# Performance work log

Measured on AMD Instinct MI355X. Metric: run time of the kernel, lower is better.

## Reference

```python
import jax, jax.numpy as jnp
import numpy as np

N, E, B = 10000, 60000, 4
NODE_IN, EDGE_IN, COND_IN, SCALE_IN = 6, 6, 10, 4
H, KW, OUT = 64, 256, 1
NUM_LAYERS = 3


def _lin(key, fan_in, fan_out):
    return jax.random.normal(key, (fan_in, fan_out), jnp.float32) / np.sqrt(fan_in).astype(np.float32)


def setup_inputs() -> dict:
    key = jax.random.key(0)
    ks = jax.random.split(key, 16)
    return {
        "x": jax.random.normal(ks[0], (N, NODE_IN), jnp.float32),
        "edge_attr": jax.random.normal(ks[1], (E, EDGE_IN), jnp.float32),
        "conditions": jax.random.normal(ks[2], (B, COND_IN), jnp.float32),
        "scale": jax.random.normal(ks[3], (B, SCALE_IN), jnp.float32),
        "edge_index": jax.random.randint(ks[4], (2, E), 0, N, dtype=jnp.int32),
        "batch": jnp.sort(jax.random.randint(ks[5], (N,), 0, B, dtype=jnp.int32)),
        # node encoder
        "nW1": _lin(ks[6], NODE_IN, H), "nb1": jnp.zeros((H,), jnp.float32),
        "nW2": _lin(ks[7], H, H), "nb2": jnp.zeros((H,), jnp.float32),
        # condition encoder
        "cW1": _lin(ks[8], COND_IN + SCALE_IN, H), "cb1": jnp.zeros((H,), jnp.float32),
        "cW2": _lin(ks[9], H, H), "cb2": jnp.zeros((H,), jnp.float32),
        # kernel network (DenseNet [EDGE_IN+H, KW//2, KW, H*H])
        "kW1": _lin(ks[10], EDGE_IN + H, KW // 2), "kb1": jnp.zeros((KW // 2,), jnp.float32),
        "kW2": _lin(ks[11], KW // 2, KW), "kb2": jnp.zeros((KW,), jnp.float32),
        "kW3": _lin(ks[12], KW, H * H), "kb3": jnp.zeros((H * H,), jnp.float32),
        # NNConv root weight + bias
        "root": _lin(ks[13], H, H), "conv_bias": jnp.zeros((H,), jnp.float32),
        # output head
        "oW": _lin(ks[14], H, OUT), "ob": jnp.zeros((OUT,), jnp.float32),
    }


def reference(x, edge_attr, conditions, scale, edge_index, batch,
              nW1, nb1, nW2, nb2, cW1, cb1, cW2, cb2,
              kW1, kb1, kW2, kb2, kW3, kb3, root, conv_bias, oW, ob):
    # node + condition encoders
    h = jax.nn.relu(x @ nW1 + nb1) @ nW2 + nb2                                   # [N,H]
    u = jax.nn.relu(jnp.concatenate([conditions, scale], 1) @ cW1 + cb1) @ cW2 + cb2  # [B,H]

    src, dst = edge_index[0], edge_index[1]
    # per-edge conditioned attributes
    ea = jnp.concatenate([edge_attr, u[batch[src]]], axis=1)                     # [E,EDGE_IN+H]
    # kernel network -> per-edge H x H weight (same every layer, compute once)
    k = jax.nn.relu(ea @ kW1 + kb1)
    k = jax.nn.relu(k @ kW2 + kb2)
    w = (k @ kW3 + kb3).reshape(E, H, H)                                          # [E,H,H]

    # mean-aggregation degree (clamped to >=1, matching scatter_mean semantics)
    deg = jnp.maximum(jax.ops.segment_sum(jnp.ones((E,), x.dtype), dst, num_segments=N), 1.0)

    for _ in range(NUM_LAYERS):
        msg = jnp.einsum('ei,eio->eo', h[src], w)                                 # gather + bmm
        agg = jax.ops.segment_sum(msg, dst, num_segments=N) / deg[:, None]        # scatter-mean
        h = jax.nn.relu(agg + h @ root + conv_bias)

    out = h @ oW + ob                                                             # [N,OUT]
    return out, u
```

## Files before the change

### kernel.cpp

```cpp
#include <hip/hip_runtime.h>
#include <hip/hip_fp16.h>

#define N_NODES 10000
#define N_EDGES 60000
#define EPAD    60032
#define CSPLIT  2
#define CT_PER  32

typedef _Float16 f16;
typedef f16 f16x8 __attribute__((ext_vector_type(8)));
typedef float f32x4 __attribute__((ext_vector_type(4)));

__device__ __forceinline__ void gload16(const void* g, void* l) {
    __builtin_amdgcn_global_load_lds((const __attribute__((address_space(1))) unsigned int*)g,
                                     (__attribute__((address_space(3))) unsigned int*)l, 16, 0, 0);
}

__device__ __forceinline__ float foldp(float a, float b, int m, int lane) {
    float x = (lane & m) ? b : a;
    float y = (lane & m) ? a : b;
    return x + __shfl_xor(y, m);
}

__global__ void k_node_enc(const float* __restrict__ x, const float* __restrict__ W1,
                           const float* __restrict__ b1, const float* __restrict__ W2,
                           const float* __restrict__ b2, float* __restrict__ h) {
    __shared__ float t[4][64];
    int g = threadIdx.x >> 6, j = threadIdx.x & 63;
    int node = blockIdx.x * 4 + g;
    float acc = b1[j];
#pragma unroll
    for (int i = 0; i < 6; ++i) acc += x[node * 6 + i] * W1[i * 64 + j];
    t[g][j] = fmaxf(acc, 0.f);
    __syncthreads();
    float acc2 = b2[j];
#pragma unroll
    for (int i = 0; i < 64; ++i) acc2 += t[g][i] * W2[i * 64 + j];
    h[node * 64 + j] = acc2;
}

__global__ void k_cond_enc(const float* __restrict__ cond, const float* __restrict__ scl,
                           const float* __restrict__ W1, const float* __restrict__ b1,
                           const float* __restrict__ W2, const float* __restrict__ b2,
                           float* __restrict__ u, float* __restrict__ out_u) {
    __shared__ float t[4][64];
    __shared__ float cat[4][14];
    int g = threadIdx.x >> 6, j = threadIdx.x & 63;
    if (threadIdx.x < 56) {
        int b = threadIdx.x / 14, i = threadIdx.x % 14;
        cat[b][i] = (i < 10) ? cond[b * 10 + i] : scl[b * 4 + (i - 10)];
    }
    __syncthreads();
    float acc = b1[j];
#pragma unroll
    for (int i = 0; i < 14; ++i) acc += cat[g][i] * W1[i * 64 + j];
    t[g][j] = fmaxf(acc, 0.f);
    __syncthreads();
    float acc2 = b2[j];
#pragma unroll
    for (int i = 0; i < 64; ++i) acc2 += t[g][i] * W2[i * 64 + j];
    u[g * 64 + j] = acc2;
    out_u[g * 64 + j] = acc2;
}

__global__ void k_deg(const int* __restrict__ dst, float* __restrict__ deg) {
    int e = blockIdx.x * 256 + threadIdx.x;
    if (e < N_EDGES) atomicAdd(&deg[dst[e]], 1.0f);
}
__global__ void k_deg_inv(float* __restrict__ deg) {
    int n = blockIdx.x * 256 + threadIdx.x;
    if (n < N_NODES) deg[n] = 1.0f / fmaxf(deg[n], 1.0f);
}

__global__ void k_permute(const float* __restrict__ kW3, const float* __restrict__ kb3,
                          f16* __restrict__ kW3P, float* __restrict__ kb3P) {
    __shared__ float T[256][65];
    int i = blockIdx.x;
    int o = threadIdx.x & 63, kq = threadIdx.x >> 6;
    for (int kk = 0; kk < 64; ++kk) {
        int k = kk * 4 + kq;
        T[k][o] = kW3[(size_t)k * 4096 + i * 64 + o];
    }
    if (threadIdx.x < 64) kb3P[threadIdx.x * 64 + i] = kb3[i * 64 + threadIdx.x];
    __syncthreads();
    int ow = threadIdx.x >> 2, kc = (threadIdx.x & 3) * 64;
    int nf = i >> 4, rl = i & 15;
    for (int c = 0; c < 8; ++c) {
        int k0 = kc + c * 8;
        int ks = k0 >> 5, kg = (k0 >> 3) & 3;
        int chunk = (nf * 8 + ks) * 64 + kg * 16 + rl;
        f16x8 v;
#pragma unroll
        for (int jj = 0; jj < 8; ++jj) v[jj] = (f16)T[k0 + jj][ow];
        *(f16x8*)(kW3P + (size_t)ow * 16384 + chunk * 8) = v;
    }
}

__global__ __launch_bounds__(256) void k_edge12(const float* __restrict__ ea, const int* __restrict__ ei,
                                                const int* __restrict__ batch, const float* __restrict__ u,
                                                const float* __restrict__ W1, const float* __restrict__ b1,
                                                const float* __restrict__ W2, const float* __restrict__ b2,
                                                f16* __restrict__ k2) {
    __shared__ float u_s[256];
    __shared__ float ea_s[16][6];
    __shared__ int b_s[16];
    __shared__ float k1_s[16][128];
    int tid = threadIdx.x;
    int e0 = blockIdx.x * 16;
    u_s[tid] = u[tid];
    if (tid < 96) {
        int e = tid / 6, i = tid % 6;
        int eg = e0 + e;
        ea_s[e][i] = (eg < N_EDGES) ? ea[(size_t)eg * 6 + i] : 0.f;
    }
    if (tid < 16) {
        int eg = e0 + tid;
        b_s[tid] = (eg < N_EDGES) ? batch[ei[eg]] : 0;
    }
    __syncthreads();
    int j = tid & 127;
#pragma unroll 1
    for (int p = 0; p < 8; ++p) {
        int e = p * 2 + (tid >> 7);
        float acc = b1[j];
#pragma unroll
        for (int i = 0; i < 6; ++i) acc += ea_s[e][i] * W1[i * 128 + j];
        const float* ur = u_s + b_s[e] * 64;
#pragma unroll
        for (int i = 0; i < 64; ++i) acc += ur[i] * W1[(6 + i) * 128 + j];
        k1_s[e][j] = fmaxf(acc, 0.f);
    }
    __syncthreads();
    float acc2[16];
#pragma unroll
    for (int e = 0; e < 16; ++e) acc2[e] = b2[tid];
    for (int i = 0; i < 128; ++i) {
        float w = W2[(size_t)i * 256 + tid];
#pragma unroll
        for (int e = 0; e < 16; ++e) acc2[e] += k1_s[e][i] * w;
    }
#pragma unroll
    for (int e = 0; e < 16; ++e) {
        int eg = e0 + e;
        k2[(size_t)eg * 256 + tid] = (f16)((eg < N_EDGES) ? fmaxf(acc2[e], 0.f) : 0.f);
    }
}

__global__ __launch_bounds__(256) void k_fused(const f16* __restrict__ A, const f16* __restrict__ Bf,
                                               const float* __restrict__ kb3P, const float* __restrict__ h,
                                               const int* __restrict__ ei, const float* __restrict__ dinv,
                                               float* __restrict__ agg) {
    __shared__ __align__(16) f16 lB[2][16384];
    __shared__ float bias_s[CT_PER * 64];
    __shared__ int src_s[128];
    __shared__ int dst_s[128];
    __shared__ float dinv_s[128];
    int tid = threadIdx.x, wave = tid >> 6, lane = tid & 63;
    int m0 = blockIdx.x * 128;
    int ct0 = blockIdx.y * CT_PER;
    if (tid < 128) {
        int eg = m0 + tid; int s = 0, d = 0; float dv = 0.f;
        if (eg < N_EDGES) { s = ei[eg]; d = ei[N_EDGES + eg]; dv = dinv[d]; }
        src_s[tid] = s; dst_s[tid] = d; dinv_s[tid] = dv;
    }
#pragma unroll
    for (int q = 0; q < CT_PER * 64 / 256; ++q)
        bias_s[q * 256 + tid] = kb3P[ct0 * 64 + q * 256 + tid];
    {
        const f16* bp = Bf + (size_t)ct0 * 16384;
#pragma unroll
        for (int q = 0; q < 8; ++q)
            gload16(bp + (q * 256 + tid) * 8, &lB[0][(q * 256 + wave * 64) * 8]);
    }
    __syncthreads();
    f16x8 a[2][8];
#pragma unroll
    for (int mf = 0; mf < 2; ++mf) {
        const f16* ap = A + (size_t)(m0 + wave * 32 + mf * 16 + (lane & 15)) * 256 + (lane >> 4) * 8;
#pragma unroll
        for (int ks = 0; ks < 8; ++ks) a[mf][ks] = *(const f16x8*)(ap + ks * 32);
    }
    float hsr[2][4][4];
#pragma unroll
    for (int mf = 0; mf < 2; ++mf)
#pragma unroll
        for (int jj = 0; jj < 4; ++jj) {
            int el = wave * 32 + mf * 16 + (lane >> 4) * 4 + jj;
            const float* hp = h + (size_t)src_s[el] * 64 + (lane & 15);
            float dv = dinv_s[el];
#pragma unroll
            for (int nf = 0; nf < 4; ++nf) hsr[mf][jj][nf] = hp[nf * 16] * dv;
        }
    int cur = 0;
    float w4[4];
#pragma unroll 1
    for (int cto = 0; cto < CT_PER; cto += 4) {
#pragma unroll
        for (int q4 = 0; q4 < 4; ++q4) {
            int ctl = cto + q4;
            if (ctl + 1 < CT_PER) {
                const f16* bp = Bf + (size_t)(ct0 + ctl + 1) * 16384;
#pragma unroll
                for (int q = 0; q < 8; ++q)
                    gload16(bp + (q * 256 + tid) * 8, &lB[cur ^ 1][(q * 256 + wave * 64) * 8]);
            }
            f32x4 acc[2][4];
#pragma unroll
            for (int nf = 0; nf < 4; ++nf) {
                float bv = bias_s[ctl * 64 + nf * 16 + (lane & 15)];
                acc[0][nf] = {bv, bv, bv, bv};
                acc[1][nf] = {bv, bv, bv, bv};
            }
            const f16* lb = lB[cur];
#pragma unroll
            for (int ks = 0; ks < 8; ++ks) {
                f16x8 bf[4];
#pragma unroll
                for (int nf = 0; nf < 4; ++nf)
                    bf[nf] = *(const f16x8*)(lb + (nf * 8 + ks) * 512 + lane * 8);
#pragma unroll
                for (int mf = 0; mf < 2; ++mf)
#pragma unroll
                    for (int nf = 0; nf < 4; ++nf)
                        acc[mf][nf] = __builtin_amdgcn_mfma_f32_16x16x32_f16(a[mf][ks], bf[nf], acc[mf][nf], 0, 0, 0);
            }
            float v[8];
#pragma unroll
            for (int mf = 0; mf < 2; ++mf)
#pragma unroll
                for (int jj = 0; jj < 4; ++jj)
                    v[mf * 4 + jj] = acc[mf][0][jj] * hsr[mf][jj][0] + acc[mf][1][jj] * hsr[mf][jj][1]
                                   + acc[mf][2][jj] * hsr[mf][jj][2] + acc[mf][3][jj] * hsr[mf][jj][3];
            float t0 = foldp(v[0], v[1], 1, lane);
            float t1 = foldp(v[2], v[3], 1, lane);
            float t2 = foldp(v[4], v[5], 1, lane);
            float t3 = foldp(v[6], v[7], 1, lane);
            float u0 = foldp(t0, t1, 2, lane);
            float u1 = foldp(t2, t3, 2, lane);
            float s0 = foldp(u0, u1, 4, lane);
            s0 += __shfl_xor(s0, 8);
            w4[q4] = s0;
            if (q4 == 3) {
                if (!(lane & 8)) {
                    int mf = (lane >> 2) & 1, jj = lane & 3;
                    int el = wave * 32 + mf * 16 + (lane >> 4) * 4 + jj;
                    float* ap2 = agg + (size_t)dst_s[el] * 64 + ct0 + cto;
                    atomicAdd(ap2 + 0, w4[0]);
                    atomicAdd(ap2 + 1, w4[1]);
                    atomicAdd(ap2 + 2, w4[2]);
                    atomicAdd(ap2 + 3, w4[3]);
                }
            }
            cur ^= 1;
            __syncthreads();
        }
    }
}

__global__ void k_update(const float* __restrict__ agg, const float* __restrict__ h,
                         const float* __restrict__ root, const float* __restrict__ bias,
                         float* __restrict__ hn) {
    __shared__ float t[4][64];
    int g = threadIdx.x >> 6, j = threadIdx.x & 63;
    int node = blockIdx.x * 4 + g;
    t[g][j] = h[node * 64 + j];
    __syncthreads();
    float acc = agg[node * 64 + j] + bias[j];
#pragma unroll
    for (int i = 0; i < 64; ++i) acc += t[g][i] * root[i * 64 + j];
    hn[node * 64 + j] = fmaxf(acc, 0.f);
}

__global__ void k_out(const float* __restrict__ h, const float* __restrict__ oW,
                      const float* __restrict__ ob, float* __restrict__ out) {
    int wg = (blockIdx.x * 256 + threadIdx.x) >> 6;
    int lane = threadIdx.x & 63;
    if (wg >= N_NODES) return;
    float p = h[wg * 64 + lane] * oW[lane];
#pragma unroll
    for (int s = 32; s > 0; s >>= 1) p += __shfl_xor(p, s);
    if (lane == 0) out[wg] = p + ob[0];
}

__global__ void k_sentinel(float* out) { out[0] = 1e30f; }

extern "C" void kernel_launch(void* const* d_in, const int* in_sizes, int n_in,
                              void* d_out, int out_size, void* d_ws, size_t ws_size,
                              hipStream_t stream) {
    const float* x          = (const float*)d_in[0];
    const float* edge_attr  = (const float*)d_in[1];
    const float* conditions = (const float*)d_in[2];
    const float* scale      = (const float*)d_in[3];
    const int*   edge_index = (const int*)d_in[4];
    const int*   batch      = (const int*)d_in[5];
    const float* nW1 = (const float*)d_in[6];  const float* nb1 = (const float*)d_in[7];
    const float* nW2 = (const float*)d_in[8];  const float* nb2 = (const float*)d_in[9];
    const float* cW1 = (const float*)d_in[10]; const float* cb1 = (const float*)d_in[11];
    const float* cW2 = (const float*)d_in[12]; const float* cb2 = (const float*)d_in[13];
    const float* kW1 = (const float*)d_in[14]; const float* kb1 = (const float*)d_in[15];
    const float* kW2 = (const float*)d_in[16]; const float* kb2 = (const float*)d_in[17];
    const float* kW3 = (const float*)d_in[18]; const float* kb3 = (const float*)d_in[19];
    const float* root = (const float*)d_in[20]; const float* conv_bias = (const float*)d_in[21];
    const float* oW  = (const float*)d_in[22]; const float* ob  = (const float*)d_in[23];
    float* out = (float*)d_out;

    char* ws = (char*)d_ws;
    size_t off = 0;
    auto alloc = [&](size_t bytes) -> char* {
        char* p = ws + off;
        off += (bytes + 255) & ~(size_t)255;
        return p;
    };
    float* h_a  = (float*)alloc((size_t)N_NODES * 64 * 4);
    float* h_b  = (float*)alloc((size_t)N_NODES * 64 * 4);
    float* agg  = (float*)alloc((size_t)N_NODES * 64 * 4);
    float* u    = (float*)alloc(256 * 4);
    float* deg  = (float*)alloc((size_t)N_NODES * 4);
    f16*   k2   = (f16*)alloc((size_t)EPAD * 256 * 2);
    f16*   kW3P = (f16*)alloc((size_t)4096 * 256 * 2);
    float* kb3P = (float*)alloc(4096 * 4);

    if (off > ws_size) {
        k_sentinel<<<1, 1, 0, stream>>>(out);
        return;
    }

    hipMemsetAsync(deg, 0, (size_t)N_NODES * 4, stream);
    k_node_enc<<<2500, 256, 0, stream>>>(x, nW1, nb1, nW2, nb2, h_a);
    k_cond_enc<<<1, 256, 0, stream>>>(conditions, scale, cW1, cb1, cW2, cb2, u, out + N_NODES);
    k_deg<<<(N_EDGES + 255) / 256, 256, 0, stream>>>(edge_index + N_EDGES, deg);
    k_deg_inv<<<(N_NODES + 255) / 256, 256, 0, stream>>>(deg);
    k_permute<<<64, 256, 0, stream>>>(kW3, kb3, kW3P, kb3P);
    k_edge12<<<EPAD / 16, 256, 0, stream>>>(edge_attr, edge_index, batch, u, kW1, kb1, kW2, kb2, k2);

    float* hc = h_a; float* hn = h_b;
    for (int l = 0; l < 3; ++l) {
        hipMemsetAsync(agg, 0, (size_t)N_NODES * 64 * 4, stream);
        k_fused<<<dim3(EPAD / 128, CSPLIT), 256, 0, stream>>>(k2, kW3P, kb3P, hc, edge_index, deg, agg);
        k_update<<<2500, 256, 0, stream>>>(agg, hc, root, conv_bias, hn);
        float* tmp = hc; hc = hn; hn = tmp;
    }
    k_out<<<2500, 256, 0, stream>>>(hc, oW, ob, out);
}
```

Measured before the change: 896.9 us.

## Halve LDS B-tile into K-halves, drop bias smem, batch atomics by eight

Reorders the permuted kW3 layout so each output column's 256-deep K range splits into two 8192-element halves. The fused edge kernel then double-buffers half-size B tiles, which halves its LDS footprint, and requests 4 blocks per CU through launch bounds. Bias is now read straight from global memory instead of being staged in shared memory. Atomics are grouped eight columns at a time rather than four. The cost is twice as many barriers per column and a register cap that may force spills.

```diff
diff --git a/kernel.cpp b/kernel.cpp
--- a/kernel.cpp
+++ b/kernel.cpp
@@ -87,12 +87,12 @@
     int nf = i >> 4, rl = i & 15;
     for (int c = 0; c < 8; ++c) {
         int k0 = kc + c * 8;
-        int ks = k0 >> 5, kg = (k0 >> 3) & 3;
-        int chunk = (nf * 8 + ks) * 64 + kg * 16 + rl;
+        int ks = k0 >> 5, kh = ks >> 2, ks4 = ks & 3, kg = (k0 >> 3) & 3;
+        size_t off = (size_t)ow * 16384 + kh * 8192 + ((nf * 4 + ks4) * 64 + kg * 16 + rl) * 8;
         f16x8 v;
 #pragma unroll
         for (int jj = 0; jj < 8; ++jj) v[jj] = (f16)T[k0 + jj][ow];
-        *(f16x8*)(kW3P + (size_t)ow * 16384 + chunk * 8) = v;
+        *(f16x8*)(kW3P + off) = v;
     }
 }
 
@@ -146,12 +146,11 @@
     }
 }
 
-__global__ __launch_bounds__(256) void k_fused(const f16* __restrict__ A, const f16* __restrict__ Bf,
-                                               const float* __restrict__ kb3P, const float* __restrict__ h,
-                                               const int* __restrict__ ei, const float* __restrict__ dinv,
-                                               float* __restrict__ agg) {
-    __shared__ __align__(16) f16 lB[2][16384];
-    __shared__ float bias_s[CT_PER * 64];
+__global__ __launch_bounds__(256, 4) void k_fused(const f16* __restrict__ A, const f16* __restrict__ Bf,
+                                                  const float* __restrict__ kb3P, const float* __restrict__ h,
+                                                  const int* __restrict__ ei, const float* __restrict__ dinv,
+                                                  float* __restrict__ agg) {
+    __shared__ __align__(16) f16 lB[2][8192];
     __shared__ int src_s[128];
     __shared__ int dst_s[128];
     __shared__ float dinv_s[128];
@@ -163,13 +162,10 @@
         if (eg < N_EDGES) { s = ei[eg]; d = ei[N_EDGES + eg]; dv = dinv[d]; }
         src_s[tid] = s; dst_s[tid] = d; dinv_s[tid] = dv;
     }
-#pragma unroll
-    for (int q = 0; q < CT_PER * 64 / 256; ++q)
-        bias_s[q * 256 + tid] = kb3P[ct0 * 64 + q * 256 + tid];
     {
-        const f16* bp = Bf + (size_t)ct0 * 16384;
-#pragma unroll
-        for (int q = 0; q < 8; ++q)
+        const f16* bp = Bf + (size_t)(ct0 * 2) * 8192;
+#pragma unroll
+        for (int q = 0; q < 4; ++q)
             gload16(bp + (q * 256 + tid) * 8, &lB[0][(q * 256 + wave * 64) * 8]);
     }
     __syncthreads();
@@ -191,38 +187,45 @@
 #pragma unroll
             for (int nf = 0; nf < 4; ++nf) hsr[mf][jj][nf] = hp[nf * 16] * dv;
         }
+    const float* bias_p = kb3P + ct0 * 64 + (lane & 15);
     int cur = 0;
-    float w4[4];
 #pragma unroll 1
-    for (int cto = 0; cto < CT_PER; cto += 4) {
-#pragma unroll
-        for (int q4 = 0; q4 < 4; ++q4) {
-            int ctl = cto + q4;
-            if (ctl + 1 < CT_PER) {
-                const f16* bp = Bf + (size_t)(ct0 + ctl + 1) * 16384;
-#pragma unroll
-                for (int q = 0; q < 8; ++q)
-                    gload16(bp + (q * 256 + tid) * 8, &lB[cur ^ 1][(q * 256 + wave * 64) * 8]);
-            }
+    for (int cto = 0; cto < CT_PER; cto += 8) {
+        float w8[8];
+#pragma unroll
+        for (int q8 = 0; q8 < 8; ++q8) {
+            int ctl = cto + q8;
             f32x4 acc[2][4];
 #pragma unroll
             for (int nf = 0; nf < 4; ++nf) {
-                float bv = bias_s[ctl * 64 + nf * 16 + (lane & 15)];
+                float bv = bias_p[ctl * 64 + nf * 16];
                 acc[0][nf] = {bv, bv, bv, bv};
                 acc[1][nf] = {bv, bv, bv, bv};
             }
-            const f16* lb = lB[cur];
-#pragma unroll
-            for (int ks = 0; ks < 8; ++ks) {
-                f16x8 bf[4];
-#pragma unroll
-                for (int nf = 0; nf < 4; ++nf)
-                    bf[nf] = *(const f16x8*)(lb + (nf * 8 + ks) * 512 + lane * 8);
-#pragma unroll
-                for (int mf = 0; mf < 2; ++mf)
+#pragma unroll
+            for (int kh = 0; kh < 2; ++kh) {
+                int seg = ctl * 2 + kh;
+                if (seg + 1 < CT_PER * 2) {
+                    const f16* bp = Bf + (size_t)(ct0 * 2 + seg + 1) * 8192;
+#pragma unroll
+                    for (int q = 0; q < 4; ++q)
+                        gload16(bp + (q * 256 + tid) * 8, &lB[cur ^ 1][(q * 256 + wave * 64) * 8]);
+                }
+                const f16* lb = lB[cur];
+#pragma unroll
+                for (int ks4 = 0; ks4 < 4; ++ks4) {
+                    f16x8 bf[4];
 #pragma unroll
                     for (int nf = 0; nf < 4; ++nf)
-                        acc[mf][nf] = __builtin_amdgcn_mfma_f32_16x16x32_f16(a[mf][ks], bf[nf], acc[mf][nf], 0, 0, 0);
+                        bf[nf] = *(const f16x8*)(lb + (nf * 4 + ks4) * 512 + lane * 8);
+#pragma unroll
+                    for (int mf = 0; mf < 2; ++mf)
+#pragma unroll
+                        for (int nf = 0; nf < 4; ++nf)
+                            acc[mf][nf] = __builtin_amdgcn_mfma_f32_16x16x32_f16(a[mf][kh * 4 + ks4], bf[nf], acc[mf][nf], 0, 0, 0);
+                }
+                cur ^= 1;
+                __syncthreads();
             }
             float v[8];
 #pragma unroll
@@ -239,20 +242,14 @@
             float u1 = foldp(t2, t3, 2, lane);
             float s0 = foldp(u0, u1, 4, lane);
             s0 += __shfl_xor(s0, 8);
-            w4[q4] = s0;
-            if (q4 == 3) {
-                if (!(lane & 8)) {
-                    int mf = (lane >> 2) & 1, jj = lane & 3;
-                    int el = wave * 32 + mf * 16 + (lane >> 4) * 4 + jj;
-                    float* ap2 = agg + (size_t)dst_s[el] * 64 + ct0 + cto;
-                    atomicAdd(ap2 + 0, w4[0]);
-                    atomicAdd(ap2 + 1, w4[1]);
-                    atomicAdd(ap2 + 2, w4[2]);
-                    atomicAdd(ap2 + 3, w4[3]);
-                }
-            }
-            cur ^= 1;
-            __syncthreads();
+            w8[q8] = s0;
+        }
+        if (!(lane & 8)) {
+            int mf = (lane >> 2) & 1, jj = lane & 3;
+            int el = wave * 32 + mf * 16 + (lane >> 4) * 4 + jj;
+            float* ap2 = agg + (size_t)dst_s[el] * 64 + ct0 + cto;
+#pragma unroll
+            for (int q8 = 0; q8 < 8; ++q8) atomicAdd(ap2 + q8, w8[q8]);
         }
     }
 }
```

Result: slower. 1.558 ms (+73.7%).

## Retile fused edge kernel to 2x2 wave grid with four column splits

Applied to the files above, without the earlier changes.

The fused edge-message kernel now splits output columns four ways instead of two, giving more blocks. Inside each block, waves form a 2x2 grid, each covering 64 edges by 32 columns rather than 32 edges by all 64 columns. This halves B-fragment LDS reads per MFMA and changes the reduction and atomic pattern. Atomics are batched in groups of eight, and bias is read from global memory instead of staged in shared memory. In exchange, each block holds more A fragments in registers and A tiles are reloaded by more column-split blocks, which raises register pressure and global traffic.

```diff
diff --git a/kernel.cpp b/kernel.cpp
--- a/kernel.cpp
+++ b/kernel.cpp
@@ -4,8 +4,8 @@
 #define N_NODES 10000
 #define N_EDGES 60000
 #define EPAD    60032
-#define CSPLIT  2
-#define CT_PER  32
+#define CSPLIT  4
+#define CT_PER  16
 
 typedef _Float16 f16;
 typedef f16 f16x8 __attribute__((ext_vector_type(8)));
@@ -151,11 +151,11 @@
                                                const int* __restrict__ ei, const float* __restrict__ dinv,
                                                float* __restrict__ agg) {
     __shared__ __align__(16) f16 lB[2][16384];
-    __shared__ float bias_s[CT_PER * 64];
     __shared__ int src_s[128];
     __shared__ int dst_s[128];
     __shared__ float dinv_s[128];
     int tid = threadIdx.x, wave = tid >> 6, lane = tid & 63;
+    int wm = wave >> 1, wn = wave & 1;
     int m0 = blockIdx.x * 128;
     int ct0 = blockIdx.y * CT_PER;
     if (tid < 128) {
@@ -163,9 +163,6 @@
         if (eg < N_EDGES) { s = ei[eg]; d = ei[N_EDGES + eg]; dv = dinv[d]; }
         src_s[tid] = s; dst_s[tid] = d; dinv_s[tid] = dv;
     }
-#pragma unroll
-    for (int q = 0; q < CT_PER * 64 / 256; ++q)
-        bias_s[q * 256 + tid] = kb3P[ct0 * 64 + q * 256 + tid];
     {
         const f16* bp = Bf + (size_t)ct0 * 16384;
 #pragma unroll
@@ -173,86 +170,83 @@
             gload16(bp + (q * 256 + tid) * 8, &lB[0][(q * 256 + wave * 64) * 8]);
     }
     __syncthreads();
-    f16x8 a[2][8];
-#pragma unroll
-    for (int mf = 0; mf < 2; ++mf) {
-        const f16* ap = A + (size_t)(m0 + wave * 32 + mf * 16 + (lane & 15)) * 256 + (lane >> 4) * 8;
+    f16x8 a[4][8];
+#pragma unroll
+    for (int mf = 0; mf < 4; ++mf) {
+        const f16* ap = A + (size_t)(m0 + wm * 64 + mf * 16 + (lane & 15)) * 256 + (lane >> 4) * 8;
 #pragma unroll
         for (int ks = 0; ks < 8; ++ks) a[mf][ks] = *(const f16x8*)(ap + ks * 32);
     }
-    float hsr[2][4][4];
-#pragma unroll
-    for (int mf = 0; mf < 2; ++mf)
+    float hsr[4][4][2];
+#pragma unroll
+    for (int mf = 0; mf < 4; ++mf)
 #pragma unroll
         for (int jj = 0; jj < 4; ++jj) {
-            int el = wave * 32 + mf * 16 + (lane >> 4) * 4 + jj;
-            const float* hp = h + (size_t)src_s[el] * 64 + (lane & 15);
+            int el = wm * 64 + mf * 16 + (lane >> 4) * 4 + jj;
+            const float* hp = h + (size_t)src_s[el] * 64 + wn * 32 + (lane & 15);
             float dv = dinv_s[el];
 #pragma unroll
-            for (int nf = 0; nf < 4; ++nf) hsr[mf][jj][nf] = hp[nf * 16] * dv;
+            for (int nf = 0; nf < 2; ++nf) hsr[mf][jj][nf] = hp[nf * 16] * dv;
         }
+    const float* bias_p = kb3P + ct0 * 64 + wn * 32 + (lane & 15);
     int cur = 0;
-    float w4[4];
 #pragma unroll 1
-    for (int cto = 0; cto < CT_PER; cto += 4) {
-#pragma unroll
-        for (int q4 = 0; q4 < 4; ++q4) {
-            int ctl = cto + q4;
+    for (int cto = 0; cto < CT_PER; cto += 8) {
+        float w8[8];
+#pragma unroll
+        for (int q8 = 0; q8 < 8; ++q8) {
+            int ctl = cto + q8;
             if (ctl + 1 < CT_PER) {
                 const f16* bp = Bf + (size_t)(ct0 + ctl + 1) * 16384;
 #pragma unroll
                 for (int q = 0; q < 8; ++q)
                     gload16(bp + (q * 256 + tid) * 8, &lB[cur ^ 1][(q * 256 + wave * 64) * 8]);
             }
-            f32x4 acc[2][4];
-#pragma unroll
-            for (int nf = 0; nf < 4; ++nf) {
-                float bv = bias_s[ctl * 64 + nf * 16 + (lane & 15)];
-                acc[0][nf] = {bv, bv, bv, bv};
-                acc[1][nf] = {bv, bv, bv, bv};
+            f32x4 acc[4][2];
+#pragma unroll
+            for (int nf = 0; nf < 2; ++nf) {
+                float bv = bias_p[ctl * 64 + nf * 16];
+#pragma unroll
+                for (int mf = 0; mf < 4; ++mf) acc[mf][nf] = {bv, bv, bv, bv};
             }
             const f16* lb = lB[cur];
 #pragma unroll
             for (int ks = 0; ks < 8; ++ks) {
-                f16x8 bf[4];
-#pragma unroll
-                for (int nf = 0; nf < 4; ++nf)
-                    bf[nf] = *(const f16x8*)(lb + (nf * 8 + ks) * 512 + lane * 8);
-#pragma unroll
-                for (int mf = 0; mf < 2; ++mf)
-#pragma unroll
-                    for (int nf = 0; nf < 4; ++nf)
+                f16x8 bf[2];
+#pragma unroll
+                for (int nf = 0; nf < 2; ++nf)
+                    bf[nf] = *(const f16x8*)(lb + ((wn * 2 + nf) * 8 + ks) * 512 + lane * 8);
+#pragma unroll
+                for (int mf = 0; mf < 4; ++mf)
+#pragma unroll
+                    for (int nf = 0; nf < 2; ++nf)
                         acc[mf][nf] = __builtin_amdgcn_mfma_f32_16x16x32_f16(a[mf][ks], bf[nf], acc[mf][nf], 0, 0, 0);
             }
-            float v[8];
-#pragma unroll
-            for (int mf = 0; mf < 2; ++mf)
+            float v[16];
+#pragma unroll
+            for (int mf = 0; mf < 4; ++mf)
 #pragma unroll
                 for (int jj = 0; jj < 4; ++jj)
-                    v[mf * 4 + jj] = acc[mf][0][jj] * hsr[mf][jj][0] + acc[mf][1][jj] * hsr[mf][jj][1]
-                                   + acc[mf][2][jj] * hsr[mf][jj][2] + acc[mf][3][jj] * hsr[mf][jj][3];
-            float t0 = foldp(v[0], v[1], 1, lane);
-            float t1 = foldp(v[2], v[3], 1, lane);
-            float t2 = foldp(v[4], v[5], 1, lane);
-            float t3 = foldp(v[6], v[7], 1, lane);
-            float u0 = foldp(t0, t1, 2, lane);
-            float u1 = foldp(t2, t3, 2, lane);
-            float s0 = foldp(u0, u1, 4, lane);
-            s0 += __shfl_xor(s0, 8);
-            w4[q4] = s0;
-            if (q4 == 3) {
-                if (!(lane & 8)) {
-                    int mf = (lane >> 2) & 1, jj = lane & 3;
-                    int el = wave * 32 + mf * 16 + (lane >> 4) * 4 + jj;
-                    float* ap2 = agg + (size_t)dst_s[el] * 64 + ct0 + cto;
-                    atomicAdd(ap2 + 0, w4[0]);
-                    atomicAdd(ap2 + 1, w4[1]);
-                    atomicAdd(ap2 + 2, w4[2]);
-                    atomicAdd(ap2 + 3, w4[3]);
-                }
-            }
+                    v[mf * 4 + jj] = acc[mf][0][jj] * hsr[mf][jj][0] + acc[mf][1][jj] * hsr[mf][jj][1];
+            float t[8];
+#pragma unroll
+            for (int i = 0; i < 8; ++i) t[i] = foldp(v[2 * i], v[2 * i + 1], 1, lane);
+            float uu[4];
+#pragma unroll
+            for (int i = 0; i < 4; ++i) uu[i] = foldp(t[2 * i], t[2 * i + 1], 2, lane);
+            float ss[2];
+#pragma unroll
+            for (int i = 0; i < 2; ++i) ss[i] = foldp(uu[2 * i], uu[2 * i + 1], 4, lane);
+            w8[q8] = foldp(ss[0], ss[1], 8, lane);
             cur ^= 1;
             __syncthreads();
+        }
+        {
+            int mf = (lane >> 2) & 3, jj = lane & 3;
+            int el = wm * 64 + mf * 16 + (lane >> 4) * 4 + jj;
+            float* ap2 = agg + (size_t)dst_s[el] * 64 + ct0 + cto;
+#pragma unroll
+            for (int q8 = 0; q8 < 8; ++q8) atomicAdd(ap2 + q8, w8[q8]);
         }
     }
 }
```

Measured after the change: 1.594 ms. +77.7%, slower.
